# Kernel optimization log

Hardware: AMD Instinct MI355X
Metric: run time of the kernel (lower is better)

## Reference

```python
import jax, jax.numpy as jnp
import numpy as np

B, L, D, NH, K, R = 2, 1024, 768, 12, 24, 768
HD = D // NH            # head_dim = 64
NFFT = 2048             # nearest power of two >= 2*L-1


def _spectral_filters():
    # Hankel matrix Z_{ij} = 2 / ((i+j)^3 - (i+j)), top-K eigvecs scaled by sigma^{1/4}
    e = np.arange(1, L + 1, dtype=np.float64)
    ipj = e[:, None] + e[None, :]
    Z = 2.0 / (ipj ** 3 - ipj)
    sigma, phi = np.linalg.eigh(Z)
    phi_k = phi[:, -K:] * (sigma[-K:] ** 0.25)
    return jnp.asarray(phi_k, dtype=jnp.float32)  # (L, K)


def setup_inputs() -> dict:
    key = jax.random.key(0)
    ks = jax.random.split(key, 16)
    s = 0.02
    lin = lambda k_, i, o: jax.random.normal(k_, (i, o), jnp.float32) * s
    return {
        "x": jax.random.normal(ks[0], (B, L, D), jnp.float32),
        "stu_filters": _spectral_filters(),
        "M_inputs": jax.random.normal(ks[1], (D, R), jnp.float32) * s,
        "M_filters": jax.random.normal(ks[2], (K, R), jnp.float32) * s,
        "wq_w": lin(ks[3], D, D), "wq_b": jnp.zeros((D,), jnp.float32),
        "wk_w": lin(ks[4], D, D), "wk_b": jnp.zeros((D,), jnp.float32),
        "wv_w": lin(ks[5], D, D), "wv_b": jnp.zeros((D,), jnp.float32),
        "wg_w": lin(ks[6], D, D), "wg_b": jnp.zeros((D,), jnp.float32),
        "wo_w": lin(ks[7], D, D), "wo_b": jnp.zeros((D,), jnp.float32),
    }


def _stu_features(x, stu_filters, M_inputs, M_filters):
    # tensordot STU path: project inputs and filters to rank R, then FFT causal conv
    u = x @ M_inputs                       # (B, L, R)
    phi = stu_filters @ M_filters          # (L, R)
    sgn = jnp.where(jnp.arange(L) % 2 == 0, 1.0, -1.0)[None, :, None]  # (1, L, 1)
    V = jnp.fft.rfft(phi, n=NFFT, axis=0)  # (NFFT//2+1, R)
    U = jnp.stack([u, u * sgn], axis=-1)   # (B, L, R, 2)
    Uf = jnp.fft.rfft(U, n=NFFT, axis=1)   # (B, NFFT//2+1, R, 2)
    conv = jnp.fft.irfft(V[None, :, :, None] * Uf, n=NFFT, axis=1)[:, :L]  # (B, L, R, 2)
    u_plus = conv[..., 0]
    u_minus = conv[..., 1] * sgn
    return u_plus + u_minus               # (B, L, R) with R == D


def reference(x, stu_filters, M_inputs, M_filters,
              wq_w, wq_b, wk_w, wk_b, wv_w, wv_b,
              wg_w, wg_b, wo_w, wo_b):
    x_tilde = _stu_features(x, stu_filters, M_inputs, M_filters)  # (B, L, D)

    heads = lambda y: y.reshape(B, L, NH, HD).transpose(0, 2, 1, 3)  # (B, H, L, h)
    q = heads(x @ wq_w + wq_b)
    k = heads(x @ wk_w + wk_b)
    v = heads(x @ wv_w + wv_b)

    # causal linear attention via cumulative outer-product state
    Z = jnp.einsum('bhtp,bhtn->bhtpn', v, k)     # (B, H, L, h, h)
    Hc = jnp.cumsum(Z, axis=2)
    Y = jnp.einsum('bhtp,bhtpn->bhtn', q, Hc)    # (B, H, L, h)
    y_attn = Y.transpose(0, 2, 1, 3).reshape(B, L, D)

    gate = jax.nn.sigmoid(x @ wg_w + wg_b)
    y = x_tilde + (y_attn - x_tilde) * gate
    return y @ wo_w + wo_b
```

## Files before the change

### kernel.cpp

```cpp
#include <hip/hip_runtime.h>
#include <math.h>

#define B_  2
#define L_  1024
#define D_  768
#define NH_ 12
#define HD_ 64
#define K_  24
#define R_  768
#define NC_ 16
#define CS_ 64

typedef __bf16 bf16x8 __attribute__((ext_vector_type(8)));
typedef float f32x4 __attribute__((ext_vector_type(4)));
typedef float f32x8 __attribute__((ext_vector_type(8)));
typedef unsigned short u16x8 __attribute__((ext_vector_type(8)));

__device__ inline unsigned short f2bf(float f) {
    union { float f; unsigned u; } v; v.f = f;
    unsigned r = v.u + 0x7FFFu + ((v.u >> 16) & 1u);
    return (unsigned short)(r >> 16);
}

__device__ inline ushort4 pack4(const f32x4 v) {
    ushort4 r;
    r.x = f2bf(v[0]); r.y = f2bf(v[1]); r.z = f2bf(v[2]); r.w = f2bf(v[3]);
    return r;
}

__device__ inline u16x8 pack8(const f32x8 v) {
    u16x8 r;
#pragma unroll
    for (int e = 0; e < 8; ++e) r[e] = f2bf(v[e]);
    return r;
}

__device__ inline f32x8 bf2f8(const u16x8 v) {
    f32x8 r;
#pragma unroll
    for (int e = 0; e < 8; ++e) {
        union { float f; unsigned u; } t;
        t.u = ((unsigned)v[e]) << 16;
        r[e] = t.f;
    }
    return r;
}

#define GLD_LDS16(g, l)                                                     \
    __builtin_amdgcn_global_load_lds(                                       \
        (const __attribute__((address_space(1))) void*)(g),                 \
        (__attribute__((address_space(3))) void*)(l), 16, 0, 0)

__global__ __launch_bounds__(256) void k_prep(const float* __restrict__ w0,
                                              const float* __restrict__ w1,
                                              const float* __restrict__ w2,
                                              const float* __restrict__ w3,
                                              const float* __restrict__ w4,
                                              const float* __restrict__ w5,
                                              unsigned short* __restrict__ Wt,
                                              const float* __restrict__ x,
                                              unsigned short* __restrict__ xb) {
    const int bid = blockIdx.x;
    const int tid = threadIdx.x;
    if (bid < 864) {
        const int z = bid / 144, rem = bid % 144;
        const float* W;
        switch (z) {
            case 0: W = w0; break;
            case 1: W = w1; break;
            case 2: W = w2; break;
            case 3: W = w3; break;
            case 4: W = w4; break;
            default: W = w5; break;
        }
        unsigned short* o = Wt + (size_t)z * D_ * D_;
        __shared__ float t[64][69];
        const int n0 = (rem % 12) * 64, k0 = (rem / 12) * 64;
        const int row = tid >> 4, c4 = (tid & 15) * 4;
#pragma unroll
        for (int i = 0; i < 4; ++i) {
            const float4 v = *reinterpret_cast<const float4*>(
                W + (size_t)(k0 + row + i * 16) * D_ + n0 + c4);
            t[row + i * 16][c4 + 0] = v.x;
            t[row + i * 16][c4 + 1] = v.y;
            t[row + i * 16][c4 + 2] = v.z;
            t[row + i * 16][c4 + 3] = v.w;
        }
        __syncthreads();
        const int orow = tid >> 4, oc4 = (tid & 15) * 4;
#pragma unroll
        for (int i = 0; i < 4; ++i) {
            const int nn = orow + i * 16;
            ushort4 o4;
            o4.x = f2bf(t[oc4 + 0][nn]);
            o4.y = f2bf(t[oc4 + 1][nn]);
            o4.z = f2bf(t[oc4 + 2][nn]);
            o4.w = f2bf(t[oc4 + 3][nn]);
            *reinterpret_cast<ushort4*>(o + (size_t)(n0 + nn) * D_ + k0 + oc4) = o4;
        }
    } else {
        const int i8 = ((bid - 864) * 256 + tid) * 8;
        float4 f0 = *reinterpret_cast<const float4*>(x + i8);
        float4 f1 = *reinterpret_cast<const float4*>(x + i8 + 4);
        u16x8 p;
        p[0] = f2bf(f0.x); p[1] = f2bf(f0.y); p[2] = f2bf(f0.z); p[3] = f2bf(f0.w);
        p[4] = f2bf(f1.x); p[5] = f2bf(f1.y); p[6] = f2bf(f1.z); p[7] = f2bf(f1.w);
        *reinterpret_cast<u16x8*>(xb + i8) = p;
    }
}

template <int FM, int FN>
__device__ __forceinline__ void gemm_core(const unsigned short* __restrict__ A,
                                          const unsigned short* __restrict__ Bt,
                                          const float* __restrict__ bias,
                                          int mode,
                                          float* __restrict__ cf,
                                          unsigned short* __restrict__ cbf,
                                          unsigned short* __restrict__ ct,
                                          int N, int Kd,
                                          int bm, int bn, int tid) {
    constexpr int BM = 2 * FM * 16;
    constexpr int BN = 2 * FN * 16;
    constexpr int CTS = BM + 4;
    __shared__ unsigned short smem[2 * BM * 64 + 2 * BN * 64];
    unsigned short (*As)[BM * 64] = (unsigned short (*)[BM * 64])smem;
    unsigned short (*Bs)[BN * 64] = (unsigned short (*)[BN * 64])(smem + 2 * BM * 64);
    const int lane = tid & 63, wave = tid >> 6;
    const int wm = (wave >> 1) * (FM * 16), wn = (wave & 1) * (FN * 16);
    const int l15 = lane & 15, lg = lane >> 4;

    f32x4 acc[FM][FN] = {};

    auto stage = [&](int buf, int k0) {
#pragma unroll
        for (int q = 0; q < FM; ++q) {
            const int s = q * 256 + tid;
            GLD_LDS16(A + (size_t)(bm + (s >> 3)) * Kd + k0 + (s & 7) * 8,
                      &As[buf][s * 8]);
        }
#pragma unroll
        for (int q = 0; q < FN; ++q) {
            const int s = q * 256 + tid;
            GLD_LDS16(Bt + (size_t)(bn + (s >> 3)) * Kd + k0 + (s & 7) * 8,
                      &Bs[buf][s * 8]);
        }
    };

    stage(0, 0);
    __syncthreads();
    int cur = 0;
    const int nt = Kd / 64;
    for (int t = 0; t < nt; ++t) {
        if (t + 1 < nt) stage(cur ^ 1, (t + 1) * 64);
#pragma unroll
        for (int ks = 0; ks < 2; ++ks) {
            const int kb = ks * 32 + lg * 8;
            bf16x8 a[FM], b[FN];
#pragma unroll
            for (int f = 0; f < FM; ++f)
                a[f] = *reinterpret_cast<const bf16x8*>(
                    &As[cur][(wm + f * 16 + l15) * 64 + kb]);
#pragma unroll
            for (int f = 0; f < FN; ++f)
                b[f] = *reinterpret_cast<const bf16x8*>(
                    &Bs[cur][(wn + f * 16 + l15) * 64 + kb]);
#pragma unroll
            for (int fm = 0; fm < FM; ++fm)
#pragma unroll
                for (int fn = 0; fn < FN; ++fn)
                    acc[fm][fn] = __builtin_amdgcn_mfma_f32_16x16x32_bf16(
                        a[fm], b[fn], acc[fm][fn], 0, 0, 0);
        }
        __syncthreads();
        cur ^= 1;
    }

#pragma unroll
    for (int fm = 0; fm < FM; ++fm)
#pragma unroll
        for (int fn = 0; fn < FN; ++fn) {
            const int cl = wn + fn * 16 + l15;
            const int col = bn + cl;
            const float bv = bias ? bias[col] : 0.f;
            const int rl = wm + fm * 16 + lg * 4;
            const int r0 = bm + rl;
            f32x4 v = acc[fm][fn];
            v[0] += bv; v[1] += bv; v[2] += bv; v[3] += bv;
            if (mode == 0) {
#pragma unroll
                for (int j = 0; j < 4; ++j)
                    cf[(size_t)(r0 + j) * N + col] = v[j];
            }
            if (mode & 1) {
#pragma unroll
                for (int j = 0; j < 4; ++j)
                    cbf[(size_t)(r0 + j) * D_ + col] = f2bf(v[j]);
            }
            if (mode & 2) {
                *reinterpret_cast<ushort4*>(&smem[cl * CTS + rl]) = pack4(v);
            }
        }

    if (mode & 2) {
        __syncthreads();
        const int bI = bm >> 10, l0 = bm & 1023;
#pragma unroll
        for (int q = 0; q < BN * BM / 8 / 256; ++q) {
            const int slot = q * 256 + tid;
            const int cl = slot / (BM / 8), seg = slot % (BM / 8);
            const int gcol = bn + cl;
            const int h = gcol >> 6, n = gcol & 63;
            *reinterpret_cast<u16x8*>(
                ct + (((size_t)bI * NH_ + h) * 64 + n) * (size_t)L_ + l0 + seg * 8) =
                *reinterpret_cast<const u16x8*>(&smem[cl * CTS + seg * 8]);
        }
    }
}

__global__ __launch_bounds__(256) void k_gemm(const unsigned short* __restrict__ A,
                                              const unsigned short* __restrict__ Bt,
                                              const float* __restrict__ bias,
                                              float* __restrict__ C,
                                              int N, int Kd) {
    gemm_core<1, 2>(A, Bt, bias, 0, C, nullptr, nullptr, N, Kd,
                    blockIdx.y * 32, blockIdx.x * 64, threadIdx.x);
}

__global__ __launch_bounds__(256) void k_gemm5(const unsigned short* __restrict__ A,
                                               const unsigned short* __restrict__ wt,
                                               const float* __restrict__ bq,
                                               const float* __restrict__ bk,
                                               const float* __restrict__ bv,
                                               const float* __restrict__ bg,
                                               unsigned short* __restrict__ ubf,
                                               unsigned short* __restrict__ qbf,
                                               unsigned short* __restrict__ ktb,
                                               unsigned short* __restrict__ vbf,
                                               unsigned short* __restrict__ vtb,
                                               unsigned short* __restrict__ gbf) {
    const int z = blockIdx.z;
    const float* bias = nullptr;
    int mode = 1;
    unsigned short* cbf = nullptr; unsigned short* ct = nullptr;
    switch (z) {
        case 0: mode = 1; cbf = ubf; bias = nullptr; break;
        case 1: mode = 1; cbf = qbf; bias = bq; break;
        case 2: mode = 2; ct = ktb; bias = bk; break;
        case 3: mode = 3; cbf = vbf; ct = vtb; bias = bv; break;
        default: mode = 1; cbf = gbf; bias = bg; break;
    }
    const unsigned short* Bt = wt + (size_t)z * D_ * D_;
    gemm_core<4, 4>(A, Bt, bias, mode, nullptr, cbf, ct, D_, D_,
                    blockIdx.y * 128, blockIdx.x * 128, threadIdx.x);
}

__global__ __launch_bounds__(256) void k_attn(const unsigned short* __restrict__ qbf,
                                              const unsigned short* __restrict__ vbf,
                                              const unsigned short* __restrict__ ktb,
                                              const unsigned short* __restrict__ vtb,
                                              unsigned short* __restrict__ yab,
                                              const float* __restrict__ F,
                                              const float* __restrict__ Mf,
                                              unsigned short* __restrict__ phiev) {
    const int tid = threadIdx.x;
    if (blockIdx.x >= 384) {
        const int idx = ((int)blockIdx.x - 384) * 256 + tid;
        const int r = idx % R_;
        const int n = idx / R_;
        float acc = 0.f;
#pragma unroll
        for (int kk = 0; kk < K_; ++kk)
            acc += F[(2 * n) * K_ + kk] * Mf[kk * R_ + r];
        phiev[idx] = f2bf(2.f * acc);
        return;
    }
    const int c = blockIdx.x & 15, h = (blockIdx.x >> 4) % NH_, b = blockIdx.x / (16 * NH_);
    __shared__ unsigned short Qs[64 * 64];
    __shared__ unsigned short Vs[64 * 64];
    __shared__ unsigned short Kc[64 * 64];
    __shared__ unsigned short Tk[2][64 * 64];
    __shared__ unsigned short Tv[2][64 * 64];
    __shared__ unsigned short Sl[64 * 72];
    __shared__ unsigned short Hl[64 * 72];

    const int lane = tid & 63, wave = tid >> 6;
    const int wr = (wave >> 1) * 32, wc = (wave & 1) * 32;
    const int l15 = lane & 15, lg = lane >> 4;

    {
        const size_t rowbase = ((size_t)(b * L_ + c * CS_)) * D_ + h * HD_;
        const size_t tbase = ((size_t)(b * NH_ + h)) * 64 * (size_t)L_ + c * 64;
#pragma unroll
        for (int q2 = 0; q2 < 2; ++q2) {
            const int s = q2 * 256 + tid;
            const int row = s >> 3, c8 = s & 7;
            GLD_LDS16(qbf + rowbase + (size_t)row * D_ + c8 * 8, &Qs[s * 8]);
            GLD_LDS16(vbf + rowbase + (size_t)row * D_ + c8 * 8, &Vs[s * 8]);
            GLD_LDS16(ktb + tbase + (size_t)row * L_ + c8 * 8, &Kc[s * 8]);
        }
    }

    auto stage_t = [&](int buf, int cc) {
        const size_t tb2 = ((size_t)(b * NH_ + h)) * 64 * (size_t)L_ + cc * 64;
#pragma unroll
        for (int q2 = 0; q2 < 2; ++q2) {
            const int s = q2 * 256 + tid;
            const int row = s >> 3, c8 = s & 7;
            GLD_LDS16(ktb + tb2 + (size_t)row * L_ + c8 * 8, &Tk[buf][s * 8]);
            GLD_LDS16(vtb + tb2 + (size_t)row * L_ + c8 * 8, &Tv[buf][s * 8]);
        }
    };

    if (c > 0) stage_t(0, 0);
    __syncthreads();

    f32x4 hacc[2][2] = {};
    int cur = 0;
    for (int cc = 0; cc < c; ++cc) {
        if (cc + 1 < c) stage_t(cur ^ 1, cc + 1);
#pragma unroll
        for (int ks = 0; ks < 2; ++ks) {
            const int kb = ks * 32 + lg * 8;
            bf16x8 av[2], bk[2];
#pragma unroll
            for (int f = 0; f < 2; ++f) {
                av[f] = *reinterpret_cast<const bf16x8*>(&Tv[cur][(wr + f * 16 + l15) * 64 + kb]);
                bk[f] = *reinterpret_cast<const bf16x8*>(&Tk[cur][(wc + f * 16 + l15) * 64 + kb]);
            }
#pragma unroll
            for (int fm = 0; fm < 2; ++fm)
#pragma unroll
                for (int fn = 0; fn < 2; ++fn)
                    hacc[fm][fn] = __builtin_amdgcn_mfma_f32_16x16x32_bf16(
                        av[fm], bk[fn], hacc[fm][fn], 0, 0, 0);
        }
        __syncthreads();
        cur ^= 1;
    }

    if (c > 0) {
#pragma unroll
        for (int fm = 0; fm < 2; ++fm)
#pragma unroll
            for (int fn = 0; fn < 2; ++fn) {
                const int n = wc + fn * 16 + l15;
                const int p0 = wr + fm * 16 + lg * 4;
                *reinterpret_cast<ushort4*>(&Hl[n * 72 + p0]) = pack4(hacc[fm][fn]);
            }
    }

    {
        f32x4 sacc[2][2] = {};
#pragma unroll
        for (int ks = 0; ks < 2; ++ks) {
            const int kb = ks * 32 + lg * 8;
            bf16x8 av[2], bq[2];
#pragma unroll
            for (int f = 0; f < 2; ++f) {
                av[f] = *reinterpret_cast<const bf16x8*>(&Vs[(wr + f * 16 + l15) * 64 + kb]);
                bq[f] = *reinterpret_cast<const bf16x8*>(&Qs[(wc + f * 16 + l15) * 64 + kb]);
            }
#pragma unroll
            for (int fm = 0; fm < 2; ++fm)
#pragma unroll
                for (int fn = 0; fn < 2; ++fn)
                    sacc[fm][fn] = __builtin_amdgcn_mfma_f32_16x16x32_bf16(
                        av[fm], bq[fn], sacc[fm][fn], 0, 0, 0);
        }
#pragma unroll
        for (int fm = 0; fm < 2; ++fm)
#pragma unroll
            for (int fn = 0; fn < 2; ++fn) {
                const int t = wc + fn * 16 + l15;
                const int s0 = wr + fm * 16 + lg * 4;
#pragma unroll
                for (int j = 0; j < 4; ++j)
                    if (s0 + j > t) sacc[fm][fn][j] = 0.f;
                *reinterpret_cast<ushort4*>(&Sl[t * 72 + s0]) = pack4(sacc[fm][fn]);
            }
    }
    __syncthreads();

    f32x4 yacc[2][2] = {};
#pragma unroll
    for (int ks = 0; ks < 2; ++ks) {
        const int kb = ks * 32 + lg * 8;
        bf16x8 ak[2], bs[2];
#pragma unroll
        for (int f = 0; f < 2; ++f) {
            ak[f] = *reinterpret_cast<const bf16x8*>(&Kc[(wr + f * 16 + l15) * 64 + kb]);
            bs[f] = *reinterpret_cast<const bf16x8*>(&Sl[(wc + f * 16 + l15) * 72 + kb]);
        }
#pragma unroll
        for (int fm = 0; fm < 2; ++fm)
#pragma unroll
            for (int fn = 0; fn < 2; ++fn)
                yacc[fm][fn] = __builtin_amdgcn_mfma_f32_16x16x32_bf16(
                    ak[fm], bs[fn], yacc[fm][fn], 0, 0, 0);
    }
    if (c > 0) {
#pragma unroll
        for (int ks = 0; ks < 2; ++ks) {
            const int kb = ks * 32 + lg * 8;
            bf16x8 ah[2], bq[2];
#pragma unroll
            for (int f = 0; f < 2; ++f) {
                ah[f] = *reinterpret_cast<const bf16x8*>(&Hl[(wr + f * 16 + l15) * 72 + kb]);
                bq[f] = *reinterpret_cast<const bf16x8*>(&Qs[(wc + f * 16 + l15) * 64 + kb]);
            }
#pragma unroll
            for (int fm = 0; fm < 2; ++fm)
#pragma unroll
                for (int fn = 0; fn < 2; ++fn)
                    yacc[fm][fn] = __builtin_amdgcn_mfma_f32_16x16x32_bf16(
                        ah[fm], bq[fn], yacc[fm][fn], 0, 0, 0);
        }
    }

#pragma unroll
    for (int fm = 0; fm < 2; ++fm)
#pragma unroll
        for (int fn = 0; fn < 2; ++fn) {
            const int n0 = wr + fm * 16 + lg * 4;
            const int t = wc + fn * 16 + l15;
            const size_t idx = ((size_t)(b * L_ + c * CS_ + t)) * D_ + h * HD_ + n0;
            *reinterpret_cast<ushort4*>(yab + idx) = pack4(yacc[fm][fn]);
        }
}

__global__ __launch_bounds__(768) void k_conv(const unsigned short* __restrict__ ubf,
                                              const unsigned short* __restrict__ phiev,
                                              const unsigned short* __restrict__ yab,
                                              const unsigned short* __restrict__ gbf,
                                              unsigned short* __restrict__ gx) {
    __shared__ u16x8 red[8][8][96];
    const int tid = threadIdx.x;
    const int g   = tid / 96;
    const int lr  = tid % 96;
    const int r   = lr * 8;
    const int m0  = blockIdx.x * 8;
    const int bp  = blockIdx.y;
    const int b   = bp >> 1, p = bp & 1;

    f32x8 acc[8] = {};
    f32x8 w[8]   = {};

    const int ns = g * 64;
    const int ne = min(ns + 64, m0 + 8);

    if (ns < ne) {
        if (g > 0) {
#pragma unroll
            for (int j = 1; j <= 7; ++j)
                w[(8 - j) & 7] = bf2f8(
                    *reinterpret_cast<const u16x8*>(phiev + (size_t)(ns - j) * R_ + r));
        }
        const unsigned short* pp = phiev + (size_t)ns * R_ + r;
        const unsigned short* up =
            ubf + ((size_t)(b * L_) + (size_t)(2 * (m0 + 7 - ns) + p)) * R_ + r;
        for (int i = ns; i < ne; i += 8) {
#pragma unroll
            for (int k = 0; k < 8; ++k) {
                const u16x8 pv = *reinterpret_cast<const u16x8*>(pp);
                const u16x8 uv = *reinterpret_cast<const u16x8*>(up);
                w[k] = bf2f8(pv);
                const f32x8 fu = bf2f8(uv);
#pragma unroll
                for (int a = 0; a < 8; ++a)
                    acc[a] += w[(k + a + 1) & 7] * fu;
                pp += R_;
                up -= 2 * R_;
            }
        }
    }

#pragma unroll
    for (int a = 0; a < 8; ++a) red[g][a][lr] = pack8(acc[a]);
    __syncthreads();

    const int a2 = tid / 96, l2 = tid % 96;
    f32x8 s = {};
#pragma unroll
    for (int g2 = 0; g2 < 8; ++g2) s += bf2f8(red[g2][a2][l2]);

    const size_t idx = ((size_t)(b * L_) + (size_t)(2 * (m0 + a2) + p)) * R_ + l2 * 8;
    const f32x8 yf = bf2f8(*reinterpret_cast<const u16x8*>(yab + idx));
    const f32x8 gf = bf2f8(*reinterpret_cast<const u16x8*>(gbf + idx));
    u16x8 o;
#pragma unroll
    for (int e = 0; e < 8; ++e) {
        const float sg = 1.f / (1.f + expf(-gf[e]));
        o[e] = f2bf(s[e] + (yf[e] - s[e]) * sg);
    }
    *reinterpret_cast<u16x8*>(gx + idx) = o;
}

extern "C" void kernel_launch(void* const* d_in, const int* in_sizes, int n_in,
                              void* d_out, int out_size, void* d_ws, size_t ws_size,
                              hipStream_t stream) {
    const float* x    = (const float*)d_in[0];
    const float* stu  = (const float*)d_in[1];
    const float* Mi   = (const float*)d_in[2];
    const float* Mf   = (const float*)d_in[3];
    const float* wq_w = (const float*)d_in[4];
    const float* wq_b = (const float*)d_in[5];
    const float* wk_w = (const float*)d_in[6];
    const float* wk_b = (const float*)d_in[7];
    const float* wv_w = (const float*)d_in[8];
    const float* wv_b = (const float*)d_in[9];
    const float* wg_w = (const float*)d_in[10];
    const float* wg_b = (const float*)d_in[11];
    const float* wo_w = (const float*)d_in[12];
    const float* wo_b = (const float*)d_in[13];
    float* out = (float*)d_out;

    char* ws = (char*)d_ws;
    size_t o = 0;
    const size_t WSZ = (size_t)D_ * D_;
    unsigned short* wbf   = (unsigned short*)(ws + o); o += 6 * WSZ * 2;
    unsigned short* xbf   = (unsigned short*)(ws + o); o += (size_t)B_ * L_ * D_ * 2;
    unsigned short* gx    = (unsigned short*)(ws + o); o += (size_t)B_ * L_ * D_ * 2;
    unsigned short* qbf   = (unsigned short*)(ws + o); o += (size_t)B_ * L_ * D_ * 2;
    unsigned short* vbf   = (unsigned short*)(ws + o); o += (size_t)B_ * L_ * D_ * 2;
    unsigned short* ubf   = (unsigned short*)(ws + o); o += (size_t)B_ * L_ * D_ * 2;
    unsigned short* gbf   = (unsigned short*)(ws + o); o += (size_t)B_ * L_ * D_ * 2;
    unsigned short* yab   = (unsigned short*)(ws + o); o += (size_t)B_ * L_ * D_ * 2;
    unsigned short* ktb   = (unsigned short*)(ws + o); o += (size_t)B_ * NH_ * 64 * L_ * 2;
    unsigned short* vtb   = (unsigned short*)(ws + o); o += (size_t)B_ * NH_ * 64 * L_ * 2;
    unsigned short* phiev = (unsigned short*)(ws + o); o += (size_t)(L_ / 2) * R_ * 2;

    unsigned short* wo_t = wbf + 5 * WSZ;

    const dim3 blk(256);

    k_prep<<<dim3(1632), blk, 0, stream>>>(Mi, wq_w, wk_w, wv_w, wg_w, wo_w, wbf,
                                           x, xbf);

    k_gemm5<<<dim3(D_ / 128, (B_ * L_) / 128, 5), blk, 0, stream>>>(
        xbf, wbf, wq_b, wk_b, wv_b, wg_b, ubf, qbf, ktb, vbf, vtb, gbf);

    k_attn<<<dim3(384 + 1536), blk, 0, stream>>>(qbf, vbf, ktb, vtb, yab,
                                                 stu, Mf, phiev);

    k_conv<<<dim3(L_ / 2 / 8, B_ * 2), dim3(768), 0, stream>>>(ubf, phiev, yab, gbf, gx);

    k_gemm<<<dim3(D_ / 64, (B_ * L_) / 32), blk, 0, stream>>>(gx, wo_t, wo_b, out, D_, D_);
}
```

Baseline: 91.94 us.

## Fuse all stages into one cooperative persistent kernel with grid syncs

Replaces the five-kernel launch sequence with a single cooperative kernel of 512 blocks that runs prep, projection GEMMs, chunked attention, spectral convolution and the output GEMM as phases separated by grid-wide syncs. The aim is to remove per-kernel launch gaps and tail effects, and shared memory is now passed in explicitly so the phases can reuse one buffer. The conv phase is re-split to fit 256-thread blocks. The cost is fixed occupancy at 512 blocks, idle blocks in the smaller phases, and the overhead of each grid sync; the old kernels remain as a fallback if the cooperative launch fails.

Result: slower. 345.7 us (+276.0%).

```diff
diff --git a/kernel.cpp b/kernel.cpp
--- a/kernel.cpp
+++ b/kernel.cpp
@@ -1,5 +1,8 @@
 #include <hip/hip_runtime.h>
+#include <hip/hip_cooperative_groups.h>
 #include <math.h>
+
+namespace cg = cooperative_groups;
 
 #define B_  2
 #define L_  1024
@@ -50,6 +53,454 @@
     __builtin_amdgcn_global_load_lds(                                       \
         (const __attribute__((address_space(1))) void*)(g),                 \
         (__attribute__((address_space(3))) void*)(l), 16, 0, 0)
+
+template <int FM, int FN>
+__device__ __forceinline__ void gemm_core(const unsigned short* __restrict__ A,
+                                          const unsigned short* __restrict__ Bt,
+                                          const float* __restrict__ bias,
+                                          int mode,
+                                          float* __restrict__ cf,
+                                          unsigned short* __restrict__ cbf,
+                                          unsigned short* __restrict__ ct,
+                                          int N, int Kd,
+                                          int bm, int bn, int tid,
+                                          unsigned short* sm) {
+    constexpr int BM = 2 * FM * 16;
+    constexpr int BN = 2 * FN * 16;
+    constexpr int CTS = BM + 4;
+    unsigned short* As0 = sm;
+    unsigned short* As1 = sm + BM * 64;
+    unsigned short* Bs0 = sm + 2 * BM * 64;
+    unsigned short* Bs1 = sm + 2 * BM * 64 + BN * 64;
+    const int lane = tid & 63, wave = tid >> 6;
+    const int wm = (wave >> 1) * (FM * 16), wn = (wave & 1) * (FN * 16);
+    const int l15 = lane & 15, lg = lane >> 4;
+
+    f32x4 acc[FM][FN] = {};
+
+    auto stage = [&](int buf, int k0) {
+        unsigned short* as = buf ? As1 : As0;
+        unsigned short* bs = buf ? Bs1 : Bs0;
+#pragma unroll
+        for (int q = 0; q < FM; ++q) {
+            const int s = q * 256 + tid;
+            GLD_LDS16(A + (size_t)(bm + (s >> 3)) * Kd + k0 + (s & 7) * 8,
+                      &as[s * 8]);
+        }
+#pragma unroll
+        for (int q = 0; q < FN; ++q) {
+            const int s = q * 256 + tid;
+            GLD_LDS16(Bt + (size_t)(bn + (s >> 3)) * Kd + k0 + (s & 7) * 8,
+                      &bs[s * 8]);
+        }
+    };
+
+    stage(0, 0);
+    __syncthreads();
+    int cur = 0;
+    const int nt = Kd / 64;
+    for (int t = 0; t < nt; ++t) {
+        if (t + 1 < nt) stage(cur ^ 1, (t + 1) * 64);
+        const unsigned short* as = cur ? As1 : As0;
+        const unsigned short* bs = cur ? Bs1 : Bs0;
+#pragma unroll
+        for (int ks = 0; ks < 2; ++ks) {
+            const int kb = ks * 32 + lg * 8;
+            bf16x8 a[FM], b[FN];
+#pragma unroll
+            for (int f = 0; f < FM; ++f)
+                a[f] = *reinterpret_cast<const bf16x8*>(&as[(wm + f * 16 + l15) * 64 + kb]);
+#pragma unroll
+            for (int f = 0; f < FN; ++f)
+                b[f] = *reinterpret_cast<const bf16x8*>(&bs[(wn + f * 16 + l15) * 64 + kb]);
+#pragma unroll
+            for (int fm = 0; fm < FM; ++fm)
+#pragma unroll
+                for (int fn = 0; fn < FN; ++fn)
+                    acc[fm][fn] = __builtin_amdgcn_mfma_f32_16x16x32_bf16(
+                        a[fm], b[fn], acc[fm][fn], 0, 0, 0);
+        }
+        __syncthreads();
+        cur ^= 1;
+    }
+
+#pragma unroll
+    for (int fm = 0; fm < FM; ++fm)
+#pragma unroll
+        for (int fn = 0; fn < FN; ++fn) {
+            const int cl = wn + fn * 16 + l15;
+            const int col = bn + cl;
+            const float bv = bias ? bias[col] : 0.f;
+            const int rl = wm + fm * 16 + lg * 4;
+            const int r0 = bm + rl;
+            f32x4 v = acc[fm][fn];
+            v[0] += bv; v[1] += bv; v[2] += bv; v[3] += bv;
+            if (mode == 0) {
+#pragma unroll
+                for (int j = 0; j < 4; ++j)
+                    cf[(size_t)(r0 + j) * N + col] = v[j];
+            }
+            if (mode & 1) {
+#pragma unroll
+                for (int j = 0; j < 4; ++j)
+                    cbf[(size_t)(r0 + j) * D_ + col] = f2bf(v[j]);
+            }
+            if (mode & 2) {
+                *reinterpret_cast<ushort4*>(&sm[cl * CTS + rl]) = pack4(v);
+            }
+        }
+
+    if (mode & 2) {
+        __syncthreads();
+        const int bI = bm >> 10, l0 = bm & 1023;
+#pragma unroll
+        for (int q = 0; q < BN * BM / 8 / 256; ++q) {
+            const int slot = q * 256 + tid;
+            const int cl = slot / (BM / 8), seg = slot % (BM / 8);
+            const int gcol = bn + cl;
+            const int h = gcol >> 6, n = gcol & 63;
+            *reinterpret_cast<u16x8*>(
+                ct + (((size_t)bI * NH_ + h) * 64 + n) * (size_t)L_ + l0 + seg * 8) =
+                *reinterpret_cast<const u16x8*>(&sm[cl * CTS + seg * 8]);
+        }
+    }
+}
+
+struct MegaArgs {
+    const float* x; const float* stu; const float* Mf;
+    const float* w0; const float* w1; const float* w2;
+    const float* w3; const float* w4; const float* w5;
+    const float* bq; const float* bk; const float* bv; const float* bg;
+    const float* bo;
+    unsigned short* wbf; unsigned short* xbf; unsigned short* gx;
+    unsigned short* qbf; unsigned short* vbf; unsigned short* ubf;
+    unsigned short* gbf; unsigned short* yab; unsigned short* ktb;
+    unsigned short* vtb; unsigned short* phiev;
+    float* out;
+};
+
+#define SMEM_BYTES 75776
+
+__global__ __launch_bounds__(256, 2) void k_mega(MegaArgs A) {
+    __shared__ __align__(16) char smem_raw[SMEM_BYTES];
+    unsigned short* sm16 = (unsigned short*)smem_raw;
+    const int bid = blockIdx.x;
+    const int tid = threadIdx.x;
+    cg::grid_group grd = cg::this_grid();
+    const size_t WSZ = (size_t)D_ * D_;
+
+    for (int u = bid; u < 3168; u += 512) {
+        if (u < 864) {
+            const int z = u / 144, rem = u % 144;
+            const float* W;
+            switch (z) {
+                case 0: W = A.w0; break;
+                case 1: W = A.w1; break;
+                case 2: W = A.w2; break;
+                case 3: W = A.w3; break;
+                case 4: W = A.w4; break;
+                default: W = A.w5; break;
+            }
+            unsigned short* o = A.wbf + (size_t)z * WSZ;
+            float (*t)[69] = (float (*)[69])smem_raw;
+            const int n0 = (rem % 12) * 64, k0 = (rem / 12) * 64;
+            const int row = tid >> 4, c4 = (tid & 15) * 4;
+            __syncthreads();
+#pragma unroll
+            for (int i = 0; i < 4; ++i) {
+                const float4 v = *reinterpret_cast<const float4*>(
+                    W + (size_t)(k0 + row + i * 16) * D_ + n0 + c4);
+                t[row + i * 16][c4 + 0] = v.x;
+                t[row + i * 16][c4 + 1] = v.y;
+                t[row + i * 16][c4 + 2] = v.z;
+                t[row + i * 16][c4 + 3] = v.w;
+            }
+            __syncthreads();
+#pragma unroll
+            for (int i = 0; i < 4; ++i) {
+                const int nn = row + i * 16;
+                ushort4 o4;
+                o4.x = f2bf(t[c4 + 0][nn]);
+                o4.y = f2bf(t[c4 + 1][nn]);
+                o4.z = f2bf(t[c4 + 2][nn]);
+                o4.w = f2bf(t[c4 + 3][nn]);
+                *reinterpret_cast<ushort4*>(o + (size_t)(n0 + nn) * D_ + k0 + c4) = o4;
+            }
+        } else if (u < 1632) {
+            const int i8 = ((u - 864) * 256 + tid) * 8;
+            float4 f0 = *reinterpret_cast<const float4*>(A.x + i8);
+            float4 f1 = *reinterpret_cast<const float4*>(A.x + i8 + 4);
+            u16x8 p;
+            p[0] = f2bf(f0.x); p[1] = f2bf(f0.y); p[2] = f2bf(f0.z); p[3] = f2bf(f0.w);
+            p[4] = f2bf(f1.x); p[5] = f2bf(f1.y); p[6] = f2bf(f1.z); p[7] = f2bf(f1.w);
+            *reinterpret_cast<u16x8*>(A.xbf + i8) = p;
+        } else {
+            const int idx = (u - 1632) * 256 + tid;
+            const int r = idx % R_;
+            const int n = idx / R_;
+            float acc = 0.f;
+#pragma unroll
+            for (int kk = 0; kk < K_; ++kk)
+                acc += A.stu[(2 * n) * K_ + kk] * A.Mf[kk * R_ + r];
+            A.phiev[idx] = f2bf(2.f * acc);
+        }
+    }
+
+    grd.sync();
+
+    if (bid < 480) {
+        const int z = bid / 96, rem = bid % 96;
+        const int bx = rem % 6, by = rem / 6;
+        const float* bias = nullptr;
+        int mode = 1;
+        unsigned short* cbf = nullptr; unsigned short* ct = nullptr;
+        switch (z) {
+            case 0: mode = 1; cbf = A.ubf; bias = nullptr; break;
+            case 1: mode = 1; cbf = A.qbf; bias = A.bq; break;
+            case 2: mode = 2; ct = A.ktb; bias = A.bk; break;
+            case 3: mode = 3; cbf = A.vbf; ct = A.vtb; bias = A.bv; break;
+            default: mode = 1; cbf = A.gbf; bias = A.bg; break;
+        }
+        gemm_core<4, 4>(A.xbf, A.wbf + (size_t)z * WSZ, bias, mode,
+                        nullptr, cbf, ct, D_, D_, by * 128, bx * 128, tid, sm16);
+    }
+
+    grd.sync();
+
+    if (bid < 384) {
+        const int c = bid & 15, h = (bid >> 4) % NH_, b = bid / (16 * NH_);
+        unsigned short* Qs  = sm16;
+        unsigned short* Vs  = sm16 + 4096;
+        unsigned short* Kc  = sm16 + 8192;
+        unsigned short* Tk0 = sm16 + 12288;
+        unsigned short* Tk1 = sm16 + 16384;
+        unsigned short* Tv0 = sm16 + 20480;
+        unsigned short* Tv1 = sm16 + 24576;
+        unsigned short* Sl  = sm16 + 28672;
+        unsigned short* Hl  = sm16 + 33280;
+
+        const int lane = tid & 63, wave = tid >> 6;
+        const int wr = (wave >> 1) * 32, wc = (wave & 1) * 32;
+        const int l15 = lane & 15, lg = lane >> 4;
+
+        {
+            const size_t rowbase = ((size_t)(b * L_ + c * CS_)) * D_ + h * HD_;
+            const size_t tbase = ((size_t)(b * NH_ + h)) * 64 * (size_t)L_ + c * 64;
+#pragma unroll
+            for (int q2 = 0; q2 < 2; ++q2) {
+                const int s = q2 * 256 + tid;
+                const int row = s >> 3, c8 = s & 7;
+                GLD_LDS16(A.qbf + rowbase + (size_t)row * D_ + c8 * 8, &Qs[s * 8]);
+                GLD_LDS16(A.vbf + rowbase + (size_t)row * D_ + c8 * 8, &Vs[s * 8]);
+                GLD_LDS16(A.ktb + tbase + (size_t)row * L_ + c8 * 8, &Kc[s * 8]);
+            }
+        }
+
+        auto stage_t = [&](int buf, int cc) {
+            unsigned short* tk = buf ? Tk1 : Tk0;
+            unsigned short* tv = buf ? Tv1 : Tv0;
+            const size_t tb2 = ((size_t)(b * NH_ + h)) * 64 * (size_t)L_ + cc * 64;
+#pragma unroll
+            for (int q2 = 0; q2 < 2; ++q2) {
+                const int s = q2 * 256 + tid;
+                const int row = s >> 3, c8 = s & 7;
+                GLD_LDS16(A.ktb + tb2 + (size_t)row * L_ + c8 * 8, &tk[s * 8]);
+                GLD_LDS16(A.vtb + tb2 + (size_t)row * L_ + c8 * 8, &tv[s * 8]);
+            }
+        };
+
+        if (c > 0) stage_t(0, 0);
+        __syncthreads();
+
+        f32x4 hacc[2][2] = {};
+        int cur = 0;
+        for (int cc = 0; cc < c; ++cc) {
+            if (cc + 1 < c) stage_t(cur ^ 1, cc + 1);
+            const unsigned short* tk = cur ? Tk1 : Tk0;
+            const unsigned short* tv = cur ? Tv1 : Tv0;
+#pragma unroll
+            for (int ks = 0; ks < 2; ++ks) {
+                const int kb = ks * 32 + lg * 8;
+                bf16x8 av[2], bk[2];
+#pragma unroll
+                for (int f = 0; f < 2; ++f) {
+                    av[f] = *reinterpret_cast<const bf16x8*>(&tv[(wr + f * 16 + l15) * 64 + kb]);
+                    bk[f] = *reinterpret_cast<const bf16x8*>(&tk[(wc + f * 16 + l15) * 64 + kb]);
+                }
+#pragma unroll
+                for (int fm = 0; fm < 2; ++fm)
+#pragma unroll
+                    for (int fn = 0; fn < 2; ++fn)
+                        hacc[fm][fn] = __builtin_amdgcn_mfma_f32_16x16x32_bf16(
+                            av[fm], bk[fn], hacc[fm][fn], 0, 0, 0);
+            }
+            __syncthreads();
+            cur ^= 1;
+        }
+
+        if (c > 0) {
+#pragma unroll
+            for (int fm = 0; fm < 2; ++fm)
+#pragma unroll
+                for (int fn = 0; fn < 2; ++fn) {
+                    const int n = wc + fn * 16 + l15;
+                    const int p0 = wr + fm * 16 + lg * 4;
+                    *reinterpret_cast<ushort4*>(&Hl[n * 72 + p0]) = pack4(hacc[fm][fn]);
+                }
+        }
+
+        {
+            f32x4 sacc[2][2] = {};
+#pragma unroll
+            for (int ks = 0; ks < 2; ++ks) {
+                const int kb = ks * 32 + lg * 8;
+                bf16x8 av[2], bq[2];
+#pragma unroll
+                for (int f = 0; f < 2; ++f) {
+                    av[f] = *reinterpret_cast<const bf16x8*>(&Vs[(wr + f * 16 + l15) * 64 + kb]);
+                    bq[f] = *reinterpret_cast<const bf16x8*>(&Qs[(wc + f * 16 + l15) * 64 + kb]);
+                }
+#pragma unroll
+                for (int fm = 0; fm < 2; ++fm)
+#pragma unroll
+                    for (int fn = 0; fn < 2; ++fn)
+                        sacc[fm][fn] = __builtin_amdgcn_mfma_f32_16x16x32_bf16(
+                            av[fm], bq[fn], sacc[fm][fn], 0, 0, 0);
+            }
+#pragma unroll
+            for (int fm = 0; fm < 2; ++fm)
+#pragma unroll
+                for (int fn = 0; fn < 2; ++fn) {
+                    const int t = wc + fn * 16 + l15;
+                    const int s0 = wr + fm * 16 + lg * 4;
+#pragma unroll
+                    for (int j = 0; j < 4; ++j)
+                        if (s0 + j > t) sacc[fm][fn][j] = 0.f;
+                    *reinterpret_cast<ushort4*>(&Sl[t * 72 + s0]) = pack4(sacc[fm][fn]);
+                }
+        }
+        __syncthreads();
+
+        f32x4 yacc[2][2] = {};
+#pragma unroll
+        for (int ks = 0; ks < 2; ++ks) {
+            const int kb = ks * 32 + lg * 8;
+            bf16x8 ak[2], bs[2];
+#pragma unroll
+            for (int f = 0; f < 2; ++f) {
+                ak[f] = *reinterpret_cast<const bf16x8*>(&Kc[(wr + f * 16 + l15) * 64 + kb]);
+                bs[f] = *reinterpret_cast<const bf16x8*>(&Sl[(wc + f * 16 + l15) * 72 + kb]);
+            }
+#pragma unroll
+            for (int fm = 0; fm < 2; ++fm)
+#pragma unroll
+                for (int fn = 0; fn < 2; ++fn)
+                    yacc[fm][fn] = __builtin_amdgcn_mfma_f32_16x16x32_bf16(
+                        ak[fm], bs[fn], yacc[fm][fn], 0, 0, 0);
+        }
+        if (c > 0) {
+#pragma unroll
+            for (int ks = 0; ks < 2; ++ks) {
+                const int kb = ks * 32 + lg * 8;
+                bf16x8 ah[2], bq[2];
+#pragma unroll
+                for (int f = 0; f < 2; ++f) {
+                    ah[f] = *reinterpret_cast<const bf16x8*>(&Hl[(wr + f * 16 + l15) * 72 + kb]);
+                    bq[f] = *reinterpret_cast<const bf16x8*>(&Qs[(wc + f * 16 + l15) * 64 + kb]);
+                }
+#pragma unroll
+                for (int fm = 0; fm < 2; ++fm)
+#pragma unroll
+                    for (int fn = 0; fn < 2; ++fn)
+                        yacc[fm][fn] = __builtin_amdgcn_mfma_f32_16x16x32_bf16(
+                            ah[fm], bq[fn], yacc[fm][fn], 0, 0, 0);
+            }
+        }
+
+#pragma unroll
+        for (int fm = 0; fm < 2; ++fm)
+#pragma unroll
+            for (int fn = 0; fn < 2; ++fn) {
+                const int n0 = wr + fm * 16 + lg * 4;
+                const int t = wc + fn * 16 + l15;
+                const size_t idx = ((size_t)(b * L_ + c * CS_ + t)) * D_ + h * HD_ + n0;
+                *reinterpret_cast<ushort4*>(A.yab + idx) = pack4(yacc[fm][fn]);
+            }
+    }
+
+    grd.sync();
+
+    if (bid < 256) {
+        const int m0 = (bid & 63) * 8;
+        const int bp = bid >> 6;
+        const int b = bp >> 1, p = bp & 1;
+        u16x8* red = (u16x8*)sm16;
+
+        if (tid < 192) {
+            const int g = tid / 96, lr = tid % 96;
+            const int r = lr * 8;
+            f32x8 acc[8] = {};
+            f32x8 w[8] = {};
+            const int ns = g * 256;
+            const int ne = min(ns + 256, m0 + 8);
+            if (ns < ne) {
+                if (g > 0) {
+#pragma unroll
+                    for (int j = 1; j <= 7; ++j)
+                        w[(8 - j) & 7] = bf2f8(*reinterpret_cast<const u16x8*>(
+                            A.phiev + (size_t)(ns - j) * R_ + r));
+                }
+                const unsigned short* pp = A.phiev + (size_t)ns * R_ + r;
+                const unsigned short* up =
+                    A.ubf + ((size_t)(b * L_) + (size_t)(2 * (m0 + 7 - ns) + p)) * R_ + r;
+                for (int i = ns; i < ne; i += 8) {
+#pragma unroll
+                    for (int k = 0; k < 8; ++k) {
+                        const u16x8 pv = *reinterpret_cast<const u16x8*>(pp);
+                        const u16x8 uv = *reinterpret_cast<const u16x8*>(up);
+                        w[k] = bf2f8(pv);
+                        const f32x8 fu = bf2f8(uv);
+#pragma unroll
+                        for (int a = 0; a < 8; ++a)
+                            acc[a] += w[(k + a + 1) & 7] * fu;
+                        pp += R_;
+                        up -= 2 * R_;
+                    }
+                }
+            }
+#pragma unroll
+            for (int a = 0; a < 8; ++a) red[(g * 8 + a) * 96 + lr] = pack8(acc[a]);
+        }
+        __syncthreads();
+
+#pragma unroll
+        for (int q = 0; q < 3; ++q) {
+            const int slot = q * 256 + tid;
+            const int a2 = slot / 96, l2 = slot % 96;
+            f32x8 s = bf2f8(red[(0 * 8 + a2) * 96 + l2]) +
+                      bf2f8(red[(1 * 8 + a2) * 96 + l2]);
+            const size_t idx =
+                ((size_t)(b * L_) + (size_t)(2 * (m0 + a2) + p)) * R_ + l2 * 8;
+            const f32x8 yf = bf2f8(*reinterpret_cast<const u16x8*>(A.yab + idx));
+            const f32x8 gf = bf2f8(*reinterpret_cast<const u16x8*>(A.gbf + idx));
+            u16x8 o;
+#pragma unroll
+            for (int e = 0; e < 8; ++e) {
+                const float sg = 1.f / (1.f + expf(-gf[e]));
+                o[e] = f2bf(s[e] + (yf[e] - s[e]) * sg);
+            }
+            *reinterpret_cast<u16x8*>(A.gx + idx) = o;
+        }
+    }
+
+    grd.sync();
+
+    if (bid < 384) {
+        const int bx = bid % 12, by = bid / 12;
+        gemm_core<2, 2>(A.gx, A.wbf + 5 * WSZ, A.bo, 0, A.out, nullptr, nullptr,
+                        D_, D_, by * 64, bx * 64, tid, sm16);
+    }
+}
 
 __global__ __launch_bounds__(256) void k_prep(const float* __restrict__ w0,
                                               const float* __restrict__ w1,
@@ -87,16 +538,15 @@
             t[row + i * 16][c4 + 3] = v.w;
         }
         __syncthreads();
-        const int orow = tid >> 4, oc4 = (tid & 15) * 4;
 #pragma unroll
         for (int i = 0; i < 4; ++i) {
-            const int nn = orow + i * 16;
+            const int nn = row + i * 16;
             ushort4 o4;
-            o4.x = f2bf(t[oc4 + 0][nn]);
-            o4.y = f2bf(t[oc4 + 1][nn]);
-            o4.z = f2bf(t[oc4 + 2][nn]);
-            o4.w = f2bf(t[oc4 + 3][nn]);
-            *reinterpret_cast<ushort4*>(o + (size_t)(n0 + nn) * D_ + k0 + oc4) = o4;
+            o4.x = f2bf(t[c4 + 0][nn]);
+            o4.y = f2bf(t[c4 + 1][nn]);
+            o4.z = f2bf(t[c4 + 2][nn]);
+            o4.w = f2bf(t[c4 + 3][nn]);
+            *reinterpret_cast<ushort4*>(o + (size_t)(n0 + nn) * D_ + k0 + c4) = o4;
         }
     } else {
         const int i8 = ((bid - 864) * 256 + tid) * 8;
@@ -107,123 +557,6 @@
         p[4] = f2bf(f1.x); p[5] = f2bf(f1.y); p[6] = f2bf(f1.z); p[7] = f2bf(f1.w);
         *reinterpret_cast<u16x8*>(xb + i8) = p;
     }
-}
-
-template <int FM, int FN>
-__device__ __forceinline__ void gemm_core(const unsigned short* __restrict__ A,
-                                          const unsigned short* __restrict__ Bt,
-                                          const float* __restrict__ bias,
-                                          int mode,
-                                          float* __restrict__ cf,
-                                          unsigned short* __restrict__ cbf,
-                                          unsigned short* __restrict__ ct,
-                                          int N, int Kd,
-                                          int bm, int bn, int tid) {
-    constexpr int BM = 2 * FM * 16;
-    constexpr int BN = 2 * FN * 16;
-    constexpr int CTS = BM + 4;
-    __shared__ unsigned short smem[2 * BM * 64 + 2 * BN * 64];
-    unsigned short (*As)[BM * 64] = (unsigned short (*)[BM * 64])smem;
-    unsigned short (*Bs)[BN * 64] = (unsigned short (*)[BN * 64])(smem + 2 * BM * 64);
-    const int lane = tid & 63, wave = tid >> 6;
-    const int wm = (wave >> 1) * (FM * 16), wn = (wave & 1) * (FN * 16);
-    const int l15 = lane & 15, lg = lane >> 4;
-
-    f32x4 acc[FM][FN] = {};
-
-    auto stage = [&](int buf, int k0) {
-#pragma unroll
-        for (int q = 0; q < FM; ++q) {
-            const int s = q * 256 + tid;
-            GLD_LDS16(A + (size_t)(bm + (s >> 3)) * Kd + k0 + (s & 7) * 8,
-                      &As[buf][s * 8]);
-        }
-#pragma unroll
-        for (int q = 0; q < FN; ++q) {
-            const int s = q * 256 + tid;
-            GLD_LDS16(Bt + (size_t)(bn + (s >> 3)) * Kd + k0 + (s & 7) * 8,
-                      &Bs[buf][s * 8]);
-        }
-    };
-
-    stage(0, 0);
-    __syncthreads();
-    int cur = 0;
-    const int nt = Kd / 64;
-    for (int t = 0; t < nt; ++t) {
-        if (t + 1 < nt) stage(cur ^ 1, (t + 1) * 64);
-#pragma unroll
-        for (int ks = 0; ks < 2; ++ks) {
-            const int kb = ks * 32 + lg * 8;
-            bf16x8 a[FM], b[FN];
-#pragma unroll
-            for (int f = 0; f < FM; ++f)
-                a[f] = *reinterpret_cast<const bf16x8*>(
-                    &As[cur][(wm + f * 16 + l15) * 64 + kb]);
-#pragma unroll
-            for (int f = 0; f < FN; ++f)
-                b[f] = *reinterpret_cast<const bf16x8*>(
-                    &Bs[cur][(wn + f * 16 + l15) * 64 + kb]);
-#pragma unroll
-            for (int fm = 0; fm < FM; ++fm)
-#pragma unroll
-                for (int fn = 0; fn < FN; ++fn)
-                    acc[fm][fn] = __builtin_amdgcn_mfma_f32_16x16x32_bf16(
-                        a[fm], b[fn], acc[fm][fn], 0, 0, 0);
-        }
-        __syncthreads();
-        cur ^= 1;
-    }
-
-#pragma unroll
-    for (int fm = 0; fm < FM; ++fm)
-#pragma unroll
-        for (int fn = 0; fn < FN; ++fn) {
-            const int cl = wn + fn * 16 + l15;
-            const int col = bn + cl;
-            const float bv = bias ? bias[col] : 0.f;
-            const int rl = wm + fm * 16 + lg * 4;
-            const int r0 = bm + rl;
-            f32x4 v = acc[fm][fn];
-            v[0] += bv; v[1] += bv; v[2] += bv; v[3] += bv;
-            if (mode == 0) {
-#pragma unroll
-                for (int j = 0; j < 4; ++j)
-                    cf[(size_t)(r0 + j) * N + col] = v[j];
-            }
-            if (mode & 1) {
-#pragma unroll
-                for (int j = 0; j < 4; ++j)
-                    cbf[(size_t)(r0 + j) * D_ + col] = f2bf(v[j]);
-            }
-            if (mode & 2) {
-                *reinterpret_cast<ushort4*>(&smem[cl * CTS + rl]) = pack4(v);
-            }
-        }
-
-    if (mode & 2) {
-        __syncthreads();
-        const int bI = bm >> 10, l0 = bm & 1023;
-#pragma unroll
-        for (int q = 0; q < BN * BM / 8 / 256; ++q) {
-            const int slot = q * 256 + tid;
-            const int cl = slot / (BM / 8), seg = slot % (BM / 8);
-            const int gcol = bn + cl;
-            const int h = gcol >> 6, n = gcol & 63;
-            *reinterpret_cast<u16x8*>(
-                ct + (((size_t)bI * NH_ + h) * 64 + n) * (size_t)L_ + l0 + seg * 8) =
-                *reinterpret_cast<const u16x8*>(&smem[cl * CTS + seg * 8]);
-        }
-    }
-}
-
-__global__ __launch_bounds__(256) void k_gemm(const unsigned short* __restrict__ A,
-                                              const unsigned short* __restrict__ Bt,
-                                              const float* __restrict__ bias,
-                                              float* __restrict__ C,
-                                              int N, int Kd) {
-    gemm_core<1, 2>(A, Bt, bias, 0, C, nullptr, nullptr, N, Kd,
-                    blockIdx.y * 32, blockIdx.x * 64, threadIdx.x);
 }
 
 __global__ __launch_bounds__(256) void k_gemm5(const unsigned short* __restrict__ A,
@@ -238,6 +571,7 @@
                                                unsigned short* __restrict__ vbf,
                                                unsigned short* __restrict__ vtb,
                                                unsigned short* __restrict__ gbf) {
+    __shared__ __align__(16) unsigned short sm[2 * 128 * 64 + 2 * 128 * 64];
     const int z = blockIdx.z;
     const float* bias = nullptr;
     int mode = 1;
@@ -249,19 +583,18 @@
         case 3: mode = 3; cbf = vbf; ct = vtb; bias = bv; break;
         default: mode = 1; cbf = gbf; bias = bg; break;
     }
-    const unsigned short* Bt = wt + (size_t)z * D_ * D_;
-    gemm_core<4, 4>(A, Bt, bias, mode, nullptr, cbf, ct, D_, D_,
-                    blockIdx.y * 128, blockIdx.x * 128, threadIdx.x);
-}
-
-__global__ __launch_bounds__(256) void k_attn(const unsigned short* __restrict__ qbf,
-                                              const unsigned short* __restrict__ vbf,
-                                              const unsigned short* __restrict__ ktb,
-                                              const unsigned short* __restrict__ vtb,
-                                              unsigned short* __restrict__ yab,
-                                              const float* __restrict__ F,
-                                              const float* __restrict__ Mf,
-                                              unsigned short* __restrict__ phiev) {
+    gemm_core<4, 4>(A, wt + (size_t)z * D_ * D_, bias, mode, nullptr, cbf, ct,
+                    D_, D_, blockIdx.y * 128, blockIdx.x * 128, threadIdx.x, sm);
+}
+
+__global__ __launch_bounds__(256) void k_attn_fb(const unsigned short* __restrict__ qbf,
+                                                 const unsigned short* __restrict__ vbf,
+                                                 const unsigned short* __restrict__ ktb,
+                                                 const unsigned short* __restrict__ vtb,
+                                                 unsigned short* __restrict__ yab,
+                                                 const float* __restrict__ F,
+                                                 const float* __restrict__ Mf,
+                                                 unsigned short* __restrict__ phiev) {
     const int tid = threadIdx.x;
     if (blockIdx.x >= 384) {
         const int idx = ((int)blockIdx.x - 384) * 256 + tid;
@@ -428,11 +761,11 @@
         }
 }
 
-__global__ __launch_bounds__(768) void k_conv(const unsigned short* __restrict__ ubf,
-                                              const unsigned short* __restrict__ phiev,
-                                              const unsigned short* __restrict__ yab,
-                                              const unsigned short* __restrict__ gbf,
-                                              unsigned short* __restrict__ gx) {
+__global__ __launch_bounds__(768) void k_conv_fb(const unsigned short* __restrict__ ubf,
+                                                 const unsigned short* __restrict__ phiev,
+                                                 const unsigned short* __restrict__ yab,
+                                                 const unsigned short* __restrict__ gbf,
+                                                 unsigned short* __restrict__ gx) {
     __shared__ u16x8 red[8][8][96];
     const int tid = threadIdx.x;
     const int g   = tid / 96;
@@ -493,6 +826,16 @@
         o[e] = f2bf(s[e] + (yf[e] - s[e]) * sg);
     }
     *reinterpret_cast<u16x8*>(gx + idx) = o;
+}
+
+__global__ __launch_bounds__(256) void k_gemm_fb(const unsigned short* __restrict__ A,
+                                                 const unsigned short* __restrict__ Bt,
+                                                 const float* __restrict__ bias,
+                                                 float* __restrict__ C,
+                                                 int N, int Kd) {
+    __shared__ __align__(16) unsigned short sm[2 * 32 * 64 + 2 * 64 * 64];
+    gemm_core<1, 2>(A, Bt, bias, 0, C, nullptr, nullptr, N, Kd,
+                    blockIdx.y * 32, blockIdx.x * 64, threadIdx.x, sm);
 }
 
 extern "C" void kernel_launch(void* const* d_in, const int* in_sizes, int n_in,
@@ -529,20 +872,33 @@
     unsigned short* vtb   = (unsigned short*)(ws + o); o += (size_t)B_ * NH_ * 64 * L_ * 2;
     unsigned short* phiev = (unsigned short*)(ws + o); o += (size_t)(L_ / 2) * R_ * 2;
 
-    unsigned short* wo_t = wbf + 5 * WSZ;
-
-    const dim3 blk(256);
-
-    k_prep<<<dim3(1632), blk, 0, stream>>>(Mi, wq_w, wk_w, wv_w, wg_w, wo_w, wbf,
-                                           x, xbf);
-
-    k_gemm5<<<dim3(D_ / 128, (B_ * L_) / 128, 5), blk, 0, stream>>>(
-        xbf, wbf, wq_b, wk_b, wv_b, wg_b, ubf, qbf, ktb, vbf, vtb, gbf);
-
-    k_attn<<<dim3(384 + 1536), blk, 0, stream>>>(qbf, vbf, ktb, vtb, yab,
-                                                 stu, Mf, phiev);
-
-    k_conv<<<dim3(L_ / 2 / 8, B_ * 2), dim3(768), 0, stream>>>(ubf, phiev, yab, gbf, gx);
-
-    k_gemm<<<dim3(D_ / 64, (B_ * L_) / 32), blk, 0, stream>>>(gx, wo_t, wo_b, out, D_, D_);
-}
+    MegaArgs margs;
+    margs.x = x; margs.stu = stu; margs.Mf = Mf;
+    margs.w0 = Mi; margs.w1 = wq_w; margs.w2 = wk_w;
+    margs.w3 = wv_w; margs.w4 = wg_w; margs.w5 = wo_w;
+    margs.bq = wq_b; margs.bk = wk_b; margs.bv = wv_b; margs.bg = wg_b;
+    margs.bo = wo_b;
+    margs.wbf = wbf; margs.xbf = xbf; margs.gx = gx;
+    margs.qbf = qbf; margs.vbf = vbf; margs.ubf = ubf;
+    margs.gbf = gbf; margs.yab = yab; margs.ktb = ktb;
+    margs.vtb = vtb; margs.phiev = phiev;
+    margs.out = out;
+
+    void* params[] = { (void*)&margs };
+    hipError_t err = hipLaunchCooperativeKernel((const void*)k_mega, dim3(512),
+                                                dim3(256), params, 0, stream);
+
+    if (err != hipSuccess) {
+        const dim3 blk(256);
+        k_prep<<<dim3(1632), blk, 0, stream>>>(Mi, wq_w, wk_w, wv_w, wg_w, wo_w,
+                                               wbf, x, xbf);
+        k_gemm5<<<dim3(D_ / 128, (B_ * L_) / 128, 5), blk, 0, stream>>>(
+            xbf, wbf, wq_b, wk_b, wv_b, wg_b, ubf, qbf, ktb, vbf, vtb, gbf);
+        k_attn_fb<<<dim3(384 + 1536), blk, 0, stream>>>(qbf, vbf, ktb, vtb, yab,
+                                                        stu, Mf, phiev);
+        k_conv_fb<<<dim3(L_ / 2 / 8, B_ * 2), dim3(768), 0, stream>>>(
+            ubf, phiev, yab, gbf, gx);
+        k_gemm_fb<<<dim3(D_ / 64, (B_ * L_) / 32), blk, 0, stream>>>(
+            gx, wbf + 5 * WSZ, wo_b, out, D_, D_);
+    }
+}
```
